# Kernel tuning notes

Hardware: AMD Instinct MI355X
Metric: run time of the kernel (lower is better)

Reference implementation:

```python
import jax, jax.numpy as jnp
import numpy as np

GRID_SIZE = 5
SPLINE_ORDER = 3
COUPLING = 0.05
LN_EPS = 1e-5
BATCH = 1024
IN_DIM = 2048
HIDDEN = [4096, 4096, 2048]


def _knots():
    k = SPLINE_ORDER
    return np.concatenate([np.full(k, -1.0), np.linspace(-1.0, 1.0, GRID_SIZE + 1), np.full(k, 1.0)])


def bspline_basis(t):
    # Replicates the module's partial in-place Cox-de Boor recursion exactly:
    # after the loops, cols[0..4] are degree-3, col 5 degree-2, col 6 degree-1, col 7 degree-0.
    knots = _knots()
    k = SPLINE_ORDER
    n = len(knots) - k - 1  # 8
    cols = [jnp.where((t >= knots[i]) & (t < knots[i + 1]), 1.0, 0.0).astype(t.dtype)
            for i in range(min(n, len(knots) - 1))]
    for degree in range(1, min(k + 1, n)):
        for i in range(n - degree):
            denom1 = knots[i + degree] - knots[i]
            denom2 = knots[i + degree + 1] - knots[i + 1]
            term1 = ((t - knots[i]) / denom1) * cols[i] if denom1 > 1e-10 else 0.0
            term2 = (((knots[i + degree + 1] - t) / denom2) * cols[i + 1]
                     if (denom2 > 1e-10 and i + 1 < n) else 0.0)
            cols[i] = term1 + term2
    return jnp.stack(cols, axis=-1)  # [..., n]


def kan_activation(x, control_points, reg_weights):
    # x: [B, D]; control_points: [D, grid+order+1]; reg_weights: [D]
    t = jnp.tanh(x)
    basis = bspline_basis(t)  # [B, D, n]
    m = min(basis.shape[-1], control_points.shape[1])  # min(8, 9) = 8
    spline = jnp.einsum('bdn,dn->bd', basis[..., :m], control_points[:, :m])
    return jnp.clip(spline * reg_weights[None, :], -10.0, 10.0)


def _generators():
    sx = np.array([[0., 1.], [1., 0.]], np.float32)
    sy = np.array([[0., -1.], [1., 0.]], np.float32)
    sz = np.array([[1., 0.], [0., -1.]], np.float32)
    return np.stack([sx, sy, sz, np.eye(2, dtype=np.float32)])  # [4,2,2]

GENS = jnp.asarray(_generators())
GEN_DIAG = jnp.asarray(np.stack([np.diagonal(g) for g in _generators()]))  # [4,2]


def noncommutative_transform(x):
    # pairs of the flattened tensor, generator index cycles mod 4
    shape = x.shape
    flat = x.reshape(-1)
    P = flat.shape[0] // 2
    vec = flat[:2 * P].reshape(P, 2)
    ng = GENS.shape[0]
    if P % ng == 0:
        v = vec.reshape(P // ng, ng, 2)                      # [Q, 4, 2]
        gv = jnp.einsum('gij,qgj->qgi', GENS, v)
        vg = v * GEN_DIAG[None, :, :]
        comm = jnp.clip(gv - vg, -1.0, 1.0)
        out = (v + COUPLING * comm).reshape(-1)
    else:
        G = GENS[jnp.arange(P) % ng]
        gv = jnp.einsum('pij,pj->pi', G, vec)
        vg = vec * jnp.diagonal(G, axis1=-2, axis2=-1)
        comm = jnp.clip(gv - vg, -1.0, 1.0)
        out = (vec + COUPLING * comm).reshape(-1)
    if flat.shape[0] % 2 == 1:
        out = jnp.concatenate([out, flat[-1:]])
    return out.reshape(shape)


def setup_inputs() -> dict:
    key = jax.random.key(0)
    ks = jax.random.split(key, 16)
    inp = {'x': jax.random.normal(ks[0], (BATCH, IN_DIM), jnp.float32)}
    prev = IN_DIM
    ncp = GRID_SIZE + SPLINE_ORDER + 1  # 9
    for li, h in enumerate(HIDDEN, start=1):
        kw, kb, kc = jax.random.split(ks[li], 3)
        inp[f'W{li}'] = jax.random.normal(kw, (h, prev), jnp.float32) / np.sqrt(prev)
        inp[f'b{li}'] = jnp.zeros((h,), jnp.float32)
        inp[f'cp{li}'] = jax.random.normal(kc, (h, ncp), jnp.float32) * 0.1
        inp[f'rw{li}'] = jnp.full((h,), 0.5, jnp.float32)
        prev = h
    inp['W_out'] = jax.random.normal(ks[10], (IN_DIM, prev), jnp.float32) / np.sqrt(prev)
    inp['b_out'] = jnp.zeros((IN_DIM,), jnp.float32)
    return inp


def reference(x, W1, b1, cp1, rw1, W2, b2, cp2, rw2, W3, b3, cp3, rw3, W_out, b_out):
    # F.layer_norm over feature dim, no affine
    mu = jnp.mean(x, axis=-1, keepdims=True)
    var = jnp.var(x, axis=-1, keepdims=True)
    cur = (x - mu) / jnp.sqrt(var + LN_EPS)
    for W, b, cp, rw in ((W1, b1, cp1, rw1), (W2, b2, cp2, rw2), (W3, b3, cp3, rw3)):
        lin = cur @ W.T + b
        kan = kan_activation(lin, cp, rw)
        cur = noncommutative_transform(kan)  # dropout = identity in eval
    return cur @ W_out.T + b_out
```

## Files before the change

kernel.cpp:

```cpp
#include <hip/hip_runtime.h>

typedef __attribute__((ext_vector_type(8))) short bf16x8;
typedef __attribute__((ext_vector_type(4))) float f32x4;

__device__ __forceinline__ float b2f(unsigned short u) {
    union { unsigned int i; float f; } x; x.i = ((unsigned int)u) << 16; return x.f;
}
__device__ __forceinline__ unsigned short f2b(float f) {
    union { float f; unsigned int i; } x; x.f = f;
    unsigned int r = x.i + 0x7fffu + ((x.i >> 16) & 1u);
    return (unsigned short)(r >> 16);
}

__device__ __forceinline__ void gl16(unsigned short* l, const unsigned short* g) {
    __builtin_amdgcn_global_load_lds((__attribute__((address_space(1))) void*)g,
                                     (__attribute__((address_space(3))) void*)l, 16, 0, 0);
}

__device__ __forceinline__ float kan_spline(float t, const float* cpf, float rwf) {
    float c3 = (t >= -1.0f && t < -0.6f) ? 1.0f : 0.0f;
    float c4 = (t >= -0.6f && t < -0.2f) ? 1.0f : 0.0f;
    float c5 = (t >= -0.2f && t <  0.2f) ? 1.0f : 0.0f;
    float c6 = (t >=  0.2f && t <  0.6f) ? 1.0f : 0.0f;
    float c7 = (t >=  0.6f && t <  1.0f) ? 1.0f : 0.0f;
    float d2 = (-0.6f - t) * 2.5f * c3;
    float d3 = (t + 1.0f) * 2.5f * c3 + (-0.2f - t) * 2.5f * c4;
    float d4 = (t + 0.6f) * 2.5f * c4 + ( 0.2f - t) * 2.5f * c5;
    float d5 = (t + 0.2f) * 2.5f * c5 + ( 0.6f - t) * 2.5f * c6;
    float d6 = (t - 0.2f) * 2.5f * c6 + ( 1.0f - t) * 2.5f * c7;
    float e1 = (-0.6f - t) * 2.5f  * d2;
    float e2 = (t + 1.0f) * 2.5f  * d2 + (-0.2f - t) * 1.25f * d3;
    float e3 = (t + 1.0f) * 1.25f * d3 + ( 0.2f - t) * 1.25f * d4;
    float e4 = (t + 0.6f) * 1.25f * d4 + ( 0.6f - t) * 1.25f * d5;
    float e5 = (t + 0.2f) * 1.25f * d5 + ( 1.0f - t) * 1.25f * d6;
    const float r12 = 1.0f / 1.2f;
    float f0 = (-0.6f - t) * 2.5f  * e1;
    float f1 = (t + 1.0f) * 2.5f  * e1 + (-0.2f - t) * 1.25f * e2;
    float f2 = (t + 1.0f) * 1.25f * e2 + ( 0.2f - t) * r12   * e3;
    float f3 = (t + 1.0f) * r12   * e3 + ( 0.6f - t) * r12   * e4;
    float f4 = (t + 0.6f) * r12   * e4 + ( 1.0f - t) * r12   * e5;
    float sp = f0*cpf[0] + f1*cpf[1] + f2*cpf[2] + f3*cpf[3] + f4*cpf[4]
             + e5*cpf[5] + d6*cpf[6] + c7*cpf[7];
    float v = sp * rwf;
    return fminf(fmaxf(v, -10.0f), 10.0f);
}

__global__ void ln_stats_kernel(const float* __restrict__ x,
                                float* __restrict__ mu, float* __restrict__ rstd) {
    const int row = blockIdx.x;
    const float* p = x + (size_t)row * 2048 + threadIdx.x * 8;
    double s = 0.0, q = 0.0;
#pragma unroll
    for (int i = 0; i < 8; ++i) { float v = p[i]; s += v; q += (double)v * v; }
    for (int o = 32; o > 0; o >>= 1) { s += __shfl_down(s, o, 64); q += __shfl_down(q, o, 64); }
    __shared__ double shs[4], shq[4];
    const int lane = threadIdx.x & 63, w = threadIdx.x >> 6;
    if (lane == 0) { shs[w] = s; shq[w] = q; }
    __syncthreads();
    if (threadIdx.x == 0) {
        double S = shs[0] + shs[1] + shs[2] + shs[3];
        double Q = shq[0] + shq[1] + shq[2] + shq[3];
        double m = S / 2048.0;
        double var = Q / 2048.0 - m * m;
        mu[row] = (float)m;
        rstd[row] = (float)(1.0 / sqrt(var + 1e-5));
    }
}

__global__ void rowsum_kernel(const float* __restrict__ W,
                              float* __restrict__ S, int K) {
    const int lane = threadIdx.x & 63, w = threadIdx.x >> 6;
    const int row = blockIdx.x * 4 + w;
    const float* p = W + (size_t)row * K;
    double s = 0.0;
    for (int c = lane * 8; c < K; c += 512) {
#pragma unroll
        for (int i = 0; i < 8; ++i) s += p[c + i];
    }
    for (int o = 32; o > 0; o >>= 1) s += __shfl_down(s, o, 64);
    if (lane == 0) S[row] = (float)s;
}

__global__ void split2_kernel(const float* __restrict__ src,
                              unsigned short* __restrict__ dst, int C) {
    const int r = blockIdx.x;
    const int c = threadIdx.x * 8;
    const float* p = src + (size_t)r * C + c;
    float4 u0 = ((const float4*)p)[0];
    float4 u1 = ((const float4*)p)[1];
    float v[8] = {u0.x, u0.y, u0.z, u0.w, u1.x, u1.y, u1.z, u1.w};
    unsigned short hi[8], lo[8];
#pragma unroll
    for (int i = 0; i < 8; ++i) {
        hi[i] = f2b(v[i]);
        lo[i] = f2b(v[i] - b2f(hi[i]));
    }
    unsigned short* d = dst + (size_t)r * 2 * C + c;
    *(uint4*)d = *(const uint4*)hi;
    *(uint4*)(d + C) = *(const uint4*)lo;
}

__global__ void cvt_kernel(const float* __restrict__ src,
                           unsigned short* __restrict__ dst) {
    const size_t i = ((size_t)blockIdx.x * 256 + threadIdx.x) * 8;
    float4 u0 = ((const float4*)(src + i))[0];
    float4 u1 = ((const float4*)(src + i))[1];
    float v[8] = {u0.x, u0.y, u0.z, u0.w, u1.x, u1.y, u1.z, u1.w};
    unsigned short t[8];
#pragma unroll
    for (int q = 0; q < 8; ++q) t[q] = f2b(v[q]);
    *(uint4*)(dst + i) = *(const uint4*)t;
}

template <int EPI>
__global__ __launch_bounds__(256, 2)
void gemm_kan2(const unsigned short* __restrict__ Ab,
               const unsigned short* __restrict__ Bb,
               const float* __restrict__ bias, const float* __restrict__ cp,
               const float* __restrict__ rw, const float* __restrict__ mu,
               const float* __restrict__ rstd, const float* __restrict__ S1,
               void* __restrict__ outp,
               int Nld, int n0, int Ktot, int lda, int ldb)
{
    constexpr int BM = 64, BN = 128, BK = 64;
    constexpr int ASZ = BM * BK;
    constexpr int BUF = ASZ + BN * BK;
    __shared__ unsigned short lds[2 * BUF];

    const int tid  = threadIdx.x;
    const int lane = tid & 63;
    const int wid  = tid >> 6;

    const int gx = gridDim.x;
    int flat = blockIdx.y * gx + blockIdx.x;
    const int nwg = gx * gridDim.y;
    if ((nwg & 7) == 0) flat = (flat & 7) * (nwg >> 3) + (flat >> 3);
    const int bm = (flat % gx) * BM;
    const int bn = (flat / gx) * BN;

    const int wmo = (wid >> 1) * 32;
    const int wno = (wid & 1) * 64;
    const int fr = lane & 15;
    const int kq = lane >> 4;

    const int uA0 = (wid << 7) + lane;
    const int uA1 = uA0 + 64;
    const int uB0 = (wid << 8) + lane;
    const size_t aoff0 = (size_t)(bm + (uA0 >> 3)) * lda + ((uA0 & 7) << 3);
    const size_t aoff1 = (size_t)(bm + (uA1 >> 3)) * lda + ((uA1 & 7) << 3);
    const size_t boff0 = (size_t)(bn + ((uB0       ) >> 3)) * ldb + ((uB0 & 7) << 3);
    const size_t boff1 = (size_t)(bn + ((uB0 +  64) >> 3)) * ldb + ((uB0 & 7) << 3);
    const size_t boff2 = (size_t)(bn + ((uB0 + 128) >> 3)) * ldb + ((uB0 & 7) << 3);
    const size_t boff3 = (size_t)(bn + ((uB0 + 192) >> 3)) * ldb + ((uB0 & 7) << 3);

    f32x4 acc[2][4] = {};

#define STAGE(BSEL, AK, BKK) do {                                     \
    unsigned short* lA_ = &lds[(BSEL) * BUF];                         \
    unsigned short* lB_ = lA_ + ASZ;                                  \
    gl16(lA_ + uA0 * 8, Ab + aoff0 + (AK));                           \
    gl16(lA_ + uA1 * 8, Ab + aoff1 + (AK));                           \
    gl16(lB_ + (uB0      ) * 8, Bb + boff0 + (BKK));                  \
    gl16(lB_ + (uB0 +  64) * 8, Bb + boff1 + (BKK));                  \
    gl16(lB_ + (uB0 + 128) * 8, Bb + boff2 + (BKK));                  \
    gl16(lB_ + (uB0 + 192) * 8, Bb + boff3 + (BKK));                  \
} while (0)

    STAGE(0, 0, 0);

    int cur = 0;
    for (int k0 = 0; k0 < Ktot; k0 += BK) {
        __syncthreads();
        if (k0 + BK < Ktot) {
            const int kn = k0 + BK;
            int ak = kn, bk = kn;
            if (EPI == 0) {
                ak = (kn < 4096) ? kn : kn - 4096;
                bk = (kn < 2048) ? kn : kn - 2048;
            }
            STAGE(cur ^ 1, ak, bk);
        }
        const unsigned short* cl = &lds[cur * BUF];
#pragma unroll
        for (int s = 0; s < 2; ++s) {
            const int cc = ((s << 2) + kq) << 3;
            bf16x8 aF[2], bF[4];
#pragma unroll
            for (int i = 0; i < 2; ++i)
                aF[i] = *(const bf16x8*)&cl[(wmo + i * 16 + fr) * BK + cc];
#pragma unroll
            for (int j = 0; j < 4; ++j)
                bF[j] = *(const bf16x8*)&cl[ASZ + (wno + j * 16 + fr) * BK + cc];
#pragma unroll
            for (int i = 0; i < 2; ++i)
#pragma unroll
                for (int j = 0; j < 4; ++j)
                    acc[i][j] = __builtin_amdgcn_mfma_f32_16x16x32_bf16(aF[i], bF[j], acc[i][j], 0, 0, 0);
        }
        cur ^= 1;
    }
#undef STAGE

    const int rowg = (lane >> 4) * 4;
#pragma unroll
    for (int j = 0; j < 4; ++j) {
        const int n = n0 + bn + wno + j * 16 + fr;
        const float bs = bias[n];
        float cpf[8], rwf = 0.0f, s1 = 0.0f;
        if (EPI < 2) {
#pragma unroll
            for (int q = 0; q < 8; ++q) cpf[q] = cp[(size_t)n * 9 + q];
            rwf = rw[n];
        }
        if (EPI == 0) s1 = S1[n];
        const int s = n & 7;
#pragma unroll
        for (int i = 0; i < 2; ++i) {
            const int m0 = bm + wmo + i * 16 + rowg;
#pragma unroll
            for (int r = 0; r < 4; ++r) {
                const int m = m0 + r;
                float v = acc[i][j][r];
                if (EPI == 0) v = (v - mu[m] * s1) * rstd[m] + bs;
                else          v += bs;
                if (EPI < 2) {
                    v = kan_spline(tanhf(v), cpf, rwf);
                    float p = __shfl_xor(v, 1, 64);
                    p = fminf(fmaxf(p, -1.0f), 1.0f);
                    if (s < 4) v += ((s == 2) ? -0.05f : 0.05f) * p;
                }
                if (EPI == 2) ((float*)outp)[(size_t)m * Nld + n] = v;
                else ((unsigned short*)outp)[(size_t)m * Nld + n] = f2b(v);
            }
        }
    }
}

template <int EPI, int BSRC>
__global__ __launch_bounds__(256, 2)
void gemm_kan(const void* __restrict__ Av, const void* __restrict__ Bv,
              const float* __restrict__ bias, const float* __restrict__ cp,
              const float* __restrict__ rw, const float* __restrict__ mu,
              const float* __restrict__ rstd, const float* __restrict__ S1,
              void* __restrict__ outp,
              int Nld, int n0, int Ktot, int lda, int ldb)
{
    constexpr int BM = 64, BN = 64, BK = 64, LDP = 72;
    constexpr bool SPL = (BSRC == 2);
    constexpr int OFF_B  = BM * LDP;
    constexpr int OFF_LO = (BM + BN) * LDP;
    __shared__ unsigned short lds[(SPL ? 2 : 1) * (BM + BN) * LDP];

    const int tid  = threadIdx.x;
    const int lane = tid & 63;
    const int wid  = tid >> 6;
    const int bm = blockIdx.x * BM;
    const int bn = blockIdx.y * BN;
    const int wmo = (wid >> 1) * 32;
    const int wno = (wid & 1) * 32;
    const int fr = lane & 15;
    const int kq = lane >> 4;
    const int sar = tid >> 3, sac = (tid & 7) << 3;
    const int sfr = tid >> 2, sfc = (tid & 3) << 4;

    f32x4 acc[2][2] = {};

    uint4 pA0 = {}, pA1 = {}, pB0 = {}, pB1 = {};
    const unsigned short* Ab = (const unsigned short*)Av;
    const unsigned short* Bb = (const unsigned short*)Bv;
    const size_t a0 = (size_t)(bm + sar) * lda + sac;
    const size_t a1 = (size_t)(bm + 32 + sar) * lda + sac;
    const size_t b0 = (size_t)(bn + sar) * ldb + sac;
    const size_t b1 = (size_t)(bn + 32 + sar) * ldb + sac;
    if constexpr (BSRC == 0) {
        pA0 = *(const uint4*)(Ab + a0);
        pA1 = *(const uint4*)(Ab + a1);
        pB0 = *(const uint4*)(Bb + b0);
        pB1 = *(const uint4*)(Bb + b1);
    }

    for (int k0 = 0; k0 < Ktot; k0 += BK) {
        if constexpr (BSRC == 0) {
            *(uint4*)&lds[sar * LDP + sac] = pA0;
            *(uint4*)&lds[(32 + sar) * LDP + sac] = pA1;
            *(uint4*)&lds[OFF_B + sar * LDP + sac] = pB0;
            *(uint4*)&lds[OFF_B + (32 + sar) * LDP + sac] = pB1;
        } else {
            {
                const float* g = (const float*)Bv + (size_t)(bn + sfr) * ldb + k0 + sfc;
                float4 u0 = ((const float4*)g)[0];
                float4 u1 = ((const float4*)g)[1];
                float4 u2 = ((const float4*)g)[2];
                float4 u3 = ((const float4*)g)[3];
                float v[16] = {u0.x,u0.y,u0.z,u0.w, u1.x,u1.y,u1.z,u1.w,
                               u2.x,u2.y,u2.z,u2.w, u3.x,u3.y,u3.z,u3.w};
                unsigned short hi[16], lo[16];
#pragma unroll
                for (int i = 0; i < 16; ++i) {
                    hi[i] = f2b(v[i]);
                    if (SPL) lo[i] = f2b(v[i] - b2f(hi[i]));
                }
                unsigned short* d = &lds[OFF_B + sfr * LDP + sfc];
                ((uint4*)d)[0] = *(const uint4*)&hi[0];
                ((uint4*)d)[1] = *(const uint4*)&hi[8];
                if constexpr (SPL) {
                    unsigned short* dl = d + OFF_LO;
                    ((uint4*)dl)[0] = *(const uint4*)&lo[0];
                    ((uint4*)dl)[1] = *(const uint4*)&lo[8];
                }
            }
            if constexpr (SPL) {
                const float* g = (const float*)Av + (size_t)(bm + sfr) * lda + k0 + sfc;
                float4 u0 = ((const float4*)g)[0];
                float4 u1 = ((const float4*)g)[1];
                float4 u2 = ((const float4*)g)[2];
                float4 u3 = ((const float4*)g)[3];
                float v[16] = {u0.x,u0.y,u0.z,u0.w, u1.x,u1.y,u1.z,u1.w,
                               u2.x,u2.y,u2.z,u2.w, u3.x,u3.y,u3.z,u3.w};
                unsigned short hi[16], lo[16];
#pragma unroll
                for (int i = 0; i < 16; ++i) {
                    hi[i] = f2b(v[i]);
                    lo[i] = f2b(v[i] - b2f(hi[i]));
                }
                unsigned short* d = &lds[sfr * LDP + sfc];
                ((uint4*)d)[0] = *(const uint4*)&hi[0];
                ((uint4*)d)[1] = *(const uint4*)&hi[8];
                unsigned short* dl = d + OFF_LO;
                ((uint4*)dl)[0] = *(const uint4*)&lo[0];
                ((uint4*)dl)[1] = *(const uint4*)&lo[8];
            } else {
                *(uint4*)&lds[sar * LDP + sac] = *(const uint4*)(Ab + a0 + k0);
                *(uint4*)&lds[(32 + sar) * LDP + sac] = *(const uint4*)(Ab + a1 + k0);
            }
        }
        __syncthreads();
        if constexpr (BSRC == 0) {
            if (k0 + BK < Ktot) {
                const int kn = k0 + BK;
                const int ak = (EPI == 0) ? (kn < 4096 ? kn : kn - 4096) : kn;
                const int bk = (EPI == 0) ? (kn < 2048 ? kn : kn - 2048) : kn;
                pA0 = *(const uint4*)(Ab + a0 + ak);
                pA1 = *(const uint4*)(Ab + a1 + ak);
                pB0 = *(const uint4*)(Bb + b0 + bk);
                pB1 = *(const uint4*)(Bb + b1 + bk);
            }
        }
#pragma unroll
        for (int s = 0; s < 2; ++s) {
            const int cc = (s * 4 + kq) << 3;
            bf16x8 aF[2], bF[2];
#pragma unroll
            for (int i = 0; i < 2; ++i)
                aF[i] = *(const bf16x8*)&lds[(wmo + i * 16 + fr) * LDP + cc];
#pragma unroll
            for (int j = 0; j < 2; ++j)
                bF[j] = *(const bf16x8*)&lds[OFF_B + (wno + j * 16 + fr) * LDP + cc];
#pragma unroll
            for (int i = 0; i < 2; ++i)
#pragma unroll
                for (int j = 0; j < 2; ++j)
                    acc[i][j] = __builtin_amdgcn_mfma_f32_16x16x32_bf16(aF[i], bF[j], acc[i][j], 0, 0, 0);
            if constexpr (SPL) {
                bf16x8 aL[2], bL[2];
#pragma unroll
                for (int i = 0; i < 2; ++i)
                    aL[i] = *(const bf16x8*)&lds[OFF_LO + (wmo + i * 16 + fr) * LDP + cc];
#pragma unroll
                for (int i = 0; i < 2; ++i)
#pragma unroll
                    for (int j = 0; j < 2; ++j)
                        acc[i][j] = __builtin_amdgcn_mfma_f32_16x16x32_bf16(aL[i], bF[j], acc[i][j], 0, 0, 0);
#pragma unroll
                for (int j = 0; j < 2; ++j)
                    bL[j] = *(const bf16x8*)&lds[OFF_LO + OFF_B + (wno + j * 16 + fr) * LDP + cc];
#pragma unroll
                for (int i = 0; i < 2; ++i)
#pragma unroll
                    for (int j = 0; j < 2; ++j)
                        acc[i][j] = __builtin_amdgcn_mfma_f32_16x16x32_bf16(aF[i], bL[j], acc[i][j], 0, 0, 0);
            }
        }
        __syncthreads();
    }

    const int rowg = (lane >> 4) * 4;
#pragma unroll
    for (int j = 0; j < 2; ++j) {
        const int n = n0 + bn + wno + j * 16 + fr;
        const float bs = bias[n];
        float cpf[8], rwf = 0.0f, s1 = 0.0f;
        if (EPI < 2) {
#pragma unroll
            for (int q = 0; q < 8; ++q) cpf[q] = cp[(size_t)n * 9 + q];
            rwf = rw[n];
        }
        if (EPI == 0) s1 = S1[n];
        const int s = n & 7;
#pragma unroll
        for (int i = 0; i < 2; ++i) {
            const int m0 = bm + wmo + i * 16 + rowg;
#pragma unroll
            for (int r = 0; r < 4; ++r) {
                const int m = m0 + r;
                float v = acc[i][j][r];
                if (EPI == 0) v = (v - mu[m] * s1) * rstd[m] + bs;
                else          v += bs;
                if (EPI < 2) {
                    v = kan_spline(tanhf(v), cpf, rwf);
                    float p = __shfl_xor(v, 1, 64);
                    p = fminf(fmaxf(p, -1.0f), 1.0f);
                    if (s < 4) v += ((s == 2) ? -0.05f : 0.05f) * p;
                }
                if (EPI == 2) ((float*)outp)[(size_t)m * Nld + n] = v;
                else ((unsigned short*)outp)[(size_t)m * Nld + n] = f2b(v);
            }
        }
    }
}

extern "C" void kernel_launch(void* const* d_in, const int* in_sizes, int n_in,
                              void* d_out, int out_size, void* d_ws, size_t ws_size,
                              hipStream_t stream) {
    const float* x    = (const float*)d_in[0];
    const float* W1   = (const float*)d_in[1];
    const float* b1   = (const float*)d_in[2];
    const float* cp1  = (const float*)d_in[3];
    const float* rw1  = (const float*)d_in[4];
    const float* W2   = (const float*)d_in[5];
    const float* b2   = (const float*)d_in[6];
    const float* cp2  = (const float*)d_in[7];
    const float* rw2  = (const float*)d_in[8];
    const float* W3   = (const float*)d_in[9];
    const float* b3   = (const float*)d_in[10];
    const float* cp3  = (const float*)d_in[11];
    const float* rw3  = (const float*)d_in[12];
    const float* Wout = (const float*)d_in[13];
    const float* bout = (const float*)d_in[14];

    char* ws = (char*)d_ws;
    float* mu   = (float*)(ws);
    float* rstd = (float*)(ws + 4096);
    float* S1   = (float*)(ws + 8192);
    unsigned short* A2 = (unsigned short*)(ws + 32768);
    unsigned short* A3 = (unsigned short*)(ws + 32768 + 8388608);
    unsigned short* A4 = A2;
    unsigned short* Asplit = A3;
    unsigned short* Wb = (unsigned short*)(ws + 32768 + 2 * 8388608);
    const size_t NEED_FULL = 32768 + 2 * 8388608 + 33554432;
    const size_t NEED_HALF = 32768 + 2 * 8388608 + 16777216;

    ln_stats_kernel<<<1024, 256, 0, stream>>>(x, mu, rstd);
    rowsum_kernel<<<1024, 256, 0, stream>>>(W1, S1, 2048);

    if (ws_size >= NEED_FULL) {
        split2_kernel<<<1024, 256, 0, stream>>>(x, Asplit, 2048);
        split2_kernel<<<4096, 256, 0, stream>>>(W1, Wb, 2048);
        gemm_kan2<0><<<dim3(16, 32), 256, 0, stream>>>(
            Asplit, Wb, b1, cp1, rw1, mu, rstd, S1, A2, 4096, 0, 6144, 4096, 4096);
        cvt_kernel<<<8192, 256, 0, stream>>>(W2, Wb);
        gemm_kan2<1><<<dim3(16, 32), 256, 0, stream>>>(
            A2, Wb, b2, cp2, rw2, nullptr, nullptr, nullptr, A3, 4096, 0, 4096, 4096, 4096);
        cvt_kernel<<<4096, 256, 0, stream>>>(W3, Wb);
        gemm_kan2<1><<<dim3(16, 16), 256, 0, stream>>>(
            A3, Wb, b3, cp3, rw3, nullptr, nullptr, nullptr, A4, 2048, 0, 4096, 4096, 4096);
        cvt_kernel<<<2048, 256, 0, stream>>>(Wout, Wb);
        gemm_kan2<2><<<dim3(16, 16), 256, 0, stream>>>(
            A4, Wb, bout, nullptr, nullptr, nullptr, nullptr, nullptr, d_out, 2048, 0, 2048, 2048, 2048);
    } else if (ws_size >= NEED_HALF) {
        split2_kernel<<<1024, 256, 0, stream>>>(x, Asplit, 2048);
        for (int h = 0; h < 2; ++h) {
            split2_kernel<<<2048, 256, 0, stream>>>(W1 + (size_t)h * 2048 * 2048, Wb, 2048);
            gemm_kan2<0><<<dim3(16, 16), 256, 0, stream>>>(
                Asplit, Wb, b1, cp1, rw1, mu, rstd, S1, A2, 4096, h * 2048, 6144, 4096, 4096);
        }
        for (int h = 0; h < 2; ++h) {
            cvt_kernel<<<4096, 256, 0, stream>>>(W2 + (size_t)h * 2048 * 4096, Wb);
            gemm_kan2<1><<<dim3(16, 16), 256, 0, stream>>>(
                A2, Wb, b2, cp2, rw2, nullptr, nullptr, nullptr, A3, 4096, h * 2048, 4096, 4096, 4096);
        }
        cvt_kernel<<<4096, 256, 0, stream>>>(W3, Wb);
        gemm_kan2<1><<<dim3(16, 16), 256, 0, stream>>>(
            A3, Wb, b3, cp3, rw3, nullptr, nullptr, nullptr, A4, 2048, 0, 4096, 4096, 4096);
        cvt_kernel<<<2048, 256, 0, stream>>>(Wout, Wb);
        gemm_kan2<2><<<dim3(16, 16), 256, 0, stream>>>(
            A4, Wb, bout, nullptr, nullptr, nullptr, nullptr, nullptr, d_out, 2048, 0, 2048, 2048, 2048);
    } else {
        gemm_kan<0, 2><<<dim3(16, 64), 256, 0, stream>>>(
            x, W1, b1, cp1, rw1, mu, rstd, S1, A2, 4096, 0, 2048, 2048, 2048);
        gemm_kan<1, 1><<<dim3(16, 64), 256, 0, stream>>>(
            A2, W2, b2, cp2, rw2, nullptr, nullptr, nullptr, A3, 4096, 0, 4096, 4096, 4096);
        gemm_kan<1, 1><<<dim3(16, 32), 256, 0, stream>>>(
            A3, W3, b3, cp3, rw3, nullptr, nullptr, nullptr, A4, 2048, 0, 4096, 4096, 4096);
        gemm_kan<2, 1><<<dim3(16, 32), 256, 0, stream>>>(
            A4, Wout, bout, nullptr, nullptr, nullptr, nullptr, nullptr, d_out, 2048, 0, 2048, 2048, 2048);
    }
}
```

Measured before the change: 449.3 us.

## Triple-buffer GEMM K-loop with XOR-swizzled LDS layout

Moves the bf16 GEMM main loop from double to triple buffering. Two stages are prefetched ahead, and an explicit vmcnt wait plus a single barrier replace the per-iteration __syncthreads. It also XOR-swizzles which 16-byte column chunk each thread loads from global memory, and reads LDS fragments with the matching swizzle, to cut bank conflicts on the ds_read of A and B tiles. The LDS footprint grows by half (72 KB per block), which may limit occupancy under launch_bounds(256,2), and the hand-written waitcnt is easy to get wrong.

```diff
diff --git a/kernel.cpp b/kernel.cpp
--- a/kernel.cpp
+++ b/kernel.cpp
@@ -125,7 +125,7 @@
     constexpr int BM = 64, BN = 128, BK = 64;
     constexpr int ASZ = BM * BK;
     constexpr int BUF = ASZ + BN * BK;
-    __shared__ unsigned short lds[2 * BUF];
+    __shared__ unsigned short lds[3 * BUF];
 
     const int tid  = threadIdx.x;
     const int lane = tid & 63;
@@ -142,16 +142,20 @@
     const int wno = (wid & 1) * 64;
     const int fr = lane & 15;
     const int kq = lane >> 4;
+    const int sxr = fr & 7;
 
     const int uA0 = (wid << 7) + lane;
     const int uA1 = uA0 + 64;
     const int uB0 = (wid << 8) + lane;
-    const size_t aoff0 = (size_t)(bm + (uA0 >> 3)) * lda + ((uA0 & 7) << 3);
-    const size_t aoff1 = (size_t)(bm + (uA1 >> 3)) * lda + ((uA1 & 7) << 3);
-    const size_t boff0 = (size_t)(bn + ((uB0       ) >> 3)) * ldb + ((uB0 & 7) << 3);
-    const size_t boff1 = (size_t)(bn + ((uB0 +  64) >> 3)) * ldb + ((uB0 & 7) << 3);
-    const size_t boff2 = (size_t)(bn + ((uB0 + 128) >> 3)) * ldb + ((uB0 & 7) << 3);
-    const size_t boff3 = (size_t)(bn + ((uB0 + 192) >> 3)) * ldb + ((uB0 & 7) << 3);
+    const int uB1 = uB0 + 64, uB2 = uB0 + 128, uB3 = uB0 + 192;
+#define SRCOL(u) (((((u) & 7) ^ (((u) >> 3) & 7))) << 3)
+    const size_t aoff0 = (size_t)(bm + (uA0 >> 3)) * lda + SRCOL(uA0);
+    const size_t aoff1 = (size_t)(bm + (uA1 >> 3)) * lda + SRCOL(uA1);
+    const size_t boff0 = (size_t)(bn + (uB0 >> 3)) * ldb + SRCOL(uB0);
+    const size_t boff1 = (size_t)(bn + (uB1 >> 3)) * ldb + SRCOL(uB1);
+    const size_t boff2 = (size_t)(bn + (uB2 >> 3)) * ldb + SRCOL(uB2);
+    const size_t boff3 = (size_t)(bn + (uB3 >> 3)) * ldb + SRCOL(uB3);
+#undef SRCOL
 
     f32x4 acc[2][4] = {};
 
@@ -160,44 +164,47 @@
     unsigned short* lB_ = lA_ + ASZ;                                  \
     gl16(lA_ + uA0 * 8, Ab + aoff0 + (AK));                           \
     gl16(lA_ + uA1 * 8, Ab + aoff1 + (AK));                           \
-    gl16(lB_ + (uB0      ) * 8, Bb + boff0 + (BKK));                  \
-    gl16(lB_ + (uB0 +  64) * 8, Bb + boff1 + (BKK));                  \
-    gl16(lB_ + (uB0 + 128) * 8, Bb + boff2 + (BKK));                  \
-    gl16(lB_ + (uB0 + 192) * 8, Bb + boff3 + (BKK));                  \
+    gl16(lB_ + uB0 * 8, Bb + boff0 + (BKK));                          \
+    gl16(lB_ + uB1 * 8, Bb + boff1 + (BKK));                          \
+    gl16(lB_ + uB2 * 8, Bb + boff2 + (BKK));                          \
+    gl16(lB_ + uB3 * 8, Bb + boff3 + (BKK));                          \
 } while (0)
 
+    const int nt = Ktot / BK;
     STAGE(0, 0, 0);
-
-    int cur = 0;
-    for (int k0 = 0; k0 < Ktot; k0 += BK) {
-        __syncthreads();
-        if (k0 + BK < Ktot) {
-            const int kn = k0 + BK;
+    STAGE(1, BK, BK);
+
+    for (int t = 0; t < nt; ++t) {
+        if (t + 1 < nt) asm volatile("s_waitcnt vmcnt(6)" ::: "memory");
+        else            asm volatile("s_waitcnt vmcnt(0)" ::: "memory");
+        __builtin_amdgcn_s_barrier();
+        __builtin_amdgcn_sched_barrier(0);
+        if (t + 2 < nt) {
+            const int kn = (t + 2) * BK;
             int ak = kn, bk = kn;
             if (EPI == 0) {
                 ak = (kn < 4096) ? kn : kn - 4096;
                 bk = (kn < 2048) ? kn : kn - 2048;
             }
-            STAGE(cur ^ 1, ak, bk);
-        }
-        const unsigned short* cl = &lds[cur * BUF];
+            STAGE((t + 2) % 3, ak, bk);
+        }
+        const unsigned short* cl = &lds[(t % 3) * BUF];
 #pragma unroll
         for (int s = 0; s < 2; ++s) {
-            const int cc = ((s << 2) + kq) << 3;
+            const int sl = ((((s << 2) + kq) ^ sxr)) << 3;
             bf16x8 aF[2], bF[4];
 #pragma unroll
             for (int i = 0; i < 2; ++i)
-                aF[i] = *(const bf16x8*)&cl[(wmo + i * 16 + fr) * BK + cc];
+                aF[i] = *(const bf16x8*)&cl[(wmo + i * 16 + fr) * BK + sl];
 #pragma unroll
             for (int j = 0; j < 4; ++j)
-                bF[j] = *(const bf16x8*)&cl[ASZ + (wno + j * 16 + fr) * BK + cc];
+                bF[j] = *(const bf16x8*)&cl[ASZ + (wno + j * 16 + fr) * BK + sl];
 #pragma unroll
             for (int i = 0; i < 2; ++i)
 #pragma unroll
                 for (int j = 0; j < 4; ++j)
                     acc[i][j] = __builtin_amdgcn_mfma_f32_16x16x32_bf16(aF[i], bF[j], acc[i][j], 0, 0, 0);
         }
-        cur ^= 1;
     }
 #undef STAGE
 
```

After: 395.8 us. 11.9% less time.
